# Kernel tuning notes

Measured on AMD Instinct MI355X. Metric: run time of the kernel, lower is better.

Reference implementation:

```python
import jax, jax.numpy as jnp
import numpy as np

T, B, N, M, H, I = 64, 256, 256, 128, 1024, 128
S = 3  # 2*shift_range + 1
EPS = 1e-8  # torch cosine_similarity eps


def setup_inputs() -> dict:
    key = jax.random.key(0)
    ks = jax.random.split(key, 24)
    def rn(k, shp, scale):
        return (jax.random.normal(k, shp) * scale).astype(jnp.float32)
    sH = 1.0 / np.sqrt(H)
    sC = 1.0 / np.sqrt(I + M)
    sM = 1.0 / np.sqrt(M)
    return {
        'x': rn(ks[0], (T, B, I), 1.0),
        # controller (ffnn): Linear(I+M -> H), stored as [in, out]
        'Wc': rn(ks[1], (I + M, H), sC), 'bc': jnp.zeros((H,), jnp.float32),
        # head params stacked: index 0 = write head, 1 = read head
        'Wk': rn(ks[2], (2, H, M), sH), 'bk': jnp.zeros((2, M), jnp.float32),
        'Wb': rn(ks[3], (2, H, 1), sH), 'bb': jnp.zeros((2, 1), jnp.float32),
        'Wg': rn(ks[4], (2, H, 1), sH), 'bg': jnp.zeros((2, 1), jnp.float32),
        'Ws': rn(ks[5], (2, H, S), sH), 'bs': jnp.zeros((2, S), jnp.float32),
        'Wgam': rn(ks[6], (2, H, 1), sH), 'bgam': jnp.zeros((2, 1), jnp.float32),
        'We': rn(ks[7], (H, M), sH), 'be': jnp.zeros((M,), jnp.float32),
        'Wa': rn(ks[8], (H, M), sH), 'ba': rn(ks[9], (M,), 1.0),
        'Wo': rn(ks[10], (M, I), sM), 'bo': jnp.zeros((I,), jnp.float32),
        # learned initial state
        'memory0': rn(ks[11], (1, N, M), 0.05),
        'ww0': rn(ks[12], (1, N), 0.05),
        'rw0': rn(ks[13], (1, N), 0.05),
        'read0': rn(ks[14], (1, M), 0.05),
    }


def reference(x, Wc, bc, Wk, bk, Wb, bb, Wg, bg, Ws, bs, Wgam, bgam,
              We, be, Wa, ba, Wo, bo, memory0, ww0, rw0, read0):
    Bb = x.shape[1]
    Nn = memory0.shape[1]

    def head(i, ht, memory, prev_w):
        k = jax.nn.relu(ht @ Wk[i] + bk[i])                      # [B, M]
        beta = jax.nn.softplus(ht @ Wb[i] + bb[i])               # [B, 1]
        g = jax.nn.sigmoid(ht @ Wg[i] + bg[i])                   # [B, 1]
        shift = jax.nn.softmax(ht @ Ws[i] + bs[i], axis=1)       # [B, S]
        gamma = jax.nn.relu(ht @ Wgam[i] + bgam[i]) + 1.0        # [B, 1]
        # content addressing: cosine similarity then sharpened softmax
        kn = jnp.maximum(jnp.linalg.norm(k, axis=-1, keepdims=True), EPS)   # [B,1]
        mn = jnp.maximum(jnp.linalg.norm(memory, axis=-1), EPS)             # [B,N]
        cos = jnp.einsum('bm,bnm->bn', k, memory) / (kn * mn)
        w = jax.nn.softmax(beta * cos, axis=1)
        # interpolation with previous weight
        w = g * w + (1.0 - g) * prev_w
        # circular convolutional shift (kernel size S=3, cross-correlation like F.conv1d)
        pad = jnp.concatenate([w[:, -1:], w, w[:, :1]], axis=1)  # [B, N+2]
        w = sum(shift[:, j:j + 1] * pad[:, j:j + Nn] for j in range(S))
        # sharpening
        w = w ** gamma
        return w / jnp.sum(w, axis=1, keepdims=True)

    mem = jnp.tile(memory0, (Bb, 1, 1))
    ww = jax.nn.softmax(jnp.tile(ww0, (Bb, 1)), axis=1)
    rw = jax.nn.softmax(jnp.tile(rw0, (Bb, 1)), axis=1)
    rd = jnp.tile(read0, (Bb, 1))

    def step(carry, xt):
        memory, ww, rw, rd = carry
        inp = jnp.concatenate([xt, rd], axis=1)
        ht = jnp.tanh(inp @ Wc + bc)                             # ffnn controller
        ww = head(0, ht, memory, ww)                             # write head
        rw = head(1, ht, memory, rw)                             # read head
        erase = jax.nn.sigmoid(ht @ We + be)                     # [B, M]
        add = jax.nn.sigmoid(ht @ Wa + ba)                       # [B, M]
        memory = memory * (1.0 - ww[:, :, None] * erase[:, None, :]) \
                 + ww[:, :, None] * add[:, None, :]
        rd = jnp.einsum('bn,bnm->bm', rw, memory)
        out = rd @ Wo + bo
        return (memory, ww, rw, rd), out

    _, ys = jax.lax.scan(step, (mem, ww, rw, rd), x)
    return ys  # [T, B, I]
```

## Files before the change

### kernel.cpp

```cpp
#include <hip/hip_runtime.h>
#include <math.h>

#define T_ 64
#define B_ 256
#define N_ 256
#define M_ 128
#define H_ 1024
#define I_ 128
#define NB 256
#define NT 512
#define MSTR 132
#define EPSF 1e-8f

#define WS_WCR  0
#define WS_W2V  131072
#define WS_WSM  (131072 + 262144)

typedef _Float16 h2_t __attribute__((ext_vector_type(2)));

__device__ __forceinline__ float fdot2(unsigned a, unsigned b, float c) {
#if __has_builtin(__builtin_amdgcn_fdot2)
  union { unsigned u; h2_t h; } ua, ub;
  ua.u = a; ub.u = b;
  return __builtin_amdgcn_fdot2(ua.h, ub.h, c, false);
#else
  union { unsigned u; _Float16 h[2]; } ua, ub;
  ua.u = a; ub.u = b;
  return c + (float)ua.h[0] * (float)ub.h[0] + (float)ua.h[1] * (float)ub.h[1];
#endif
}

__device__ __forceinline__ unsigned packh2(float a, float b) {
  union { h2_t h; unsigned u; } v;
  v.h = h2_t{(_Float16)a, (_Float16)b};
  return v.u;
}

__device__ __forceinline__ float wave_rsum(float v) {
#pragma unroll
  for (int o = 32; o > 0; o >>= 1) v += __shfl_xor(v, o, 64);
  return v;
}
__device__ __forceinline__ float wave_rmax(float v) {
#pragma unroll
  for (int o = 32; o > 0; o >>= 1) v = fmaxf(v, __shfl_xor(v, o, 64));
  return v;
}

__global__ void ntm_pack(const float* __restrict__ Wc, const float* __restrict__ Wk,
                         const float* __restrict__ Wb, const float* __restrict__ Wg,
                         const float* __restrict__ Wsf, const float* __restrict__ Wgm,
                         const float* __restrict__ We, const float* __restrict__ Wa,
                         unsigned* __restrict__ wsu)
{
  const int total = 131072 + 262144 + 6144;
  for (int i = blockIdx.x * blockDim.x + threadIdx.x; i < total;
       i += gridDim.x * blockDim.x) {
    if (i < 131072) {
      int u = i;
      int k8 = u >> 12, rem = u & 4095, h = rem >> 2, jm = rem & 3;
      int j = k8 * 4 + jm;
      wsu[WS_WCR + u] = packh2(Wc[(size_t)j * H_ + h], Wc[(size_t)(j + 128) * H_ + h]);
    } else if (i < 131072 + 262144) {
      int u = i - 131072;
      int k8 = u >> 11, rem = u & 2047, c = rem >> 2, jm = rem & 3;
      int h = k8 * 4 + jm;
      float v0, v1;
      if (c < 128)      { v0 = Wk[(size_t)h * M_ + c];             v1 = Wk[(size_t)(h + 512) * M_ + c]; }
      else if (c < 256) { v0 = Wk[(size_t)H_ * M_ + (size_t)h * M_ + (c - 128)];
                          v1 = Wk[(size_t)H_ * M_ + (size_t)(h + 512) * M_ + (c - 128)]; }
      else if (c < 384) { v0 = We[(size_t)h * M_ + (c - 256)];     v1 = We[(size_t)(h + 512) * M_ + (c - 256)]; }
      else              { v0 = Wa[(size_t)h * M_ + (c - 384)];     v1 = Wa[(size_t)(h + 512) * M_ + (c - 384)]; }
      wsu[WS_W2V + u] = packh2(v0, v1);
    } else {
      int u = i - 131072 - 262144;
      int d = u >> 9, j = u & 511;
      float v0, v1;
      if (d < 2)      { v0 = Wb[d * H_ + j];        v1 = Wb[d * H_ + j + 512]; }
      else if (d < 4) { v0 = Wg[(d - 2) * H_ + j];  v1 = Wg[(d - 2) * H_ + j + 512]; }
      else if (d < 6) { v0 = Wgm[(d - 4) * H_ + j]; v1 = Wgm[(d - 4) * H_ + j + 512]; }
      else if (d < 9) { v0 = Wsf[j * 3 + (d - 6)];  v1 = Wsf[(j + 512) * 3 + (d - 6)]; }
      else            { v0 = Wsf[3 * H_ + j * 3 + (d - 9)]; v1 = Wsf[3 * H_ + (j + 512) * 3 + (d - 9)]; }
      wsu[WS_WSM + u] = packh2(v0, v1);
    }
  }
}

__global__ __launch_bounds__(NT)
void ntm_main(const float* __restrict__ x,
              const float* __restrict__ bc,  const float* __restrict__ bk,
              const float* __restrict__ bbv, const float* __restrict__ bg,
              const float* __restrict__ bsf, const float* __restrict__ bgm,
              const float* __restrict__ be,  const float* __restrict__ ba,
              const float* __restrict__ Wo,  const float* __restrict__ bo,
              const float* __restrict__ mem0, const float* __restrict__ ww0,
              const float* __restrict__ rw0,  const float* __restrict__ rd0,
              const unsigned* __restrict__ wsu,
              float* __restrict__ out)
{
  __shared__ __align__(16) float mem[N_ * MSTR];
  __shared__ __align__(16) float hts[H_];
  __shared__ __align__(16) unsigned htp[512];
  __shared__ __align__(16) unsigned inpp[128];
  __shared__ __align__(16) float prevw[2 * N_];
  __shared__ __align__(16) float mnv[N_];
  __shared__ __align__(16) float ksh[2 * M_];
  __shared__ __align__(16) float eah[2 * M_];
  __shared__ __align__(16) float wlog[2 * N_];
  __shared__ __align__(16) float wtmp[2 * N_];
  __shared__ __align__(16) float red[2 * N_];
  __shared__ __align__(16) float red2[2 * N_];
  __shared__ __align__(16) float rds[M_];
  __shared__ __align__(16) float scal[32];
  __shared__ __align__(16) float bcL[H_];
  __shared__ __align__(16) float bkL[256];
  __shared__ __align__(16) float beL[128];
  __shared__ __align__(16) float baL[128];
  __shared__ __align__(16) float boL[128];
  __shared__ __align__(16) float sb[16];

  const int tid = threadIdx.x;
  const int b = blockIdx.x;
  const uint4* WcR4 = (const uint4*)(wsu + WS_WCR);
  const uint4* W2v4 = (const uint4*)(wsu + WS_W2V);
  const uint4* Wsm4 = (const uint4*)(wsu + WS_WSM);
  const uint4* ip4 = (const uint4*)inpp;
  const uint4* hp4 = (const uint4*)htp;

  for (int i = tid; i < N_ * M_; i += NT)
    mem[(i >> 7) * MSTR + (i & 127)] = mem0[i];
  for (int i = tid; i < H_; i += NT) bcL[i] = bc[i];
  if (tid < 256) bkL[tid] = bk[tid];
  if (tid < 128) { beL[tid] = be[tid]; baL[tid] = ba[tid]; boL[tid] = bo[tid]; rds[tid] = rd0[tid]; }
  if (tid < 12) {
    float v;
    if (tid < 2) v = bbv[tid];
    else if (tid < 4) v = bg[tid - 2];
    else if (tid < 6) v = bgm[tid - 4];
    else v = bsf[tid - 6];
    sb[tid] = v;
  }
  if (tid < 256) { wlog[tid] = ww0[tid]; wlog[256 + tid] = rw0[tid]; }
  __syncthreads();
  if (tid < 256) {
    float s = 0.f;
#pragma unroll 8
    for (int m = 0; m < M_; ++m) { float v = mem[tid * MSTR + m]; s += v * v; }
    mnv[tid] = fmaxf(sqrtf(s), EPSF);
  }
  __syncthreads();
  {
    int wv = tid >> 6, ln = tid & 63;
    if (wv < 2) {
      float l0 = wlog[wv * N_ + ln], l1 = wlog[wv * N_ + 64 + ln],
            l2 = wlog[wv * N_ + 128 + ln], l3 = wlog[wv * N_ + 192 + ln];
      float mx = wave_rmax(fmaxf(fmaxf(l0, l1), fmaxf(l2, l3)));
      float e0 = __expf(l0 - mx), e1 = __expf(l1 - mx), e2 = __expf(l2 - mx), e3 = __expf(l3 - mx);
      float sm = wave_rsum(e0 + e1 + e2 + e3);
      wlog[wv * N_ + ln] = e0; wlog[wv * N_ + 64 + ln] = e1;
      wlog[wv * N_ + 128 + ln] = e2; wlog[wv * N_ + 192 + ln] = e3;
      if (ln == 0) scal[30 + wv] = 1.f / sm;
    }
  }
  __syncthreads();
  prevw[tid] = wlog[tid] * scal[30 + (tid >> 8)];
  if (tid < 128) inpp[tid] = packh2(x[(size_t)b * I_ + tid], rds[tid]);
  __syncthreads();

  for (int t = 0; t < T_; ++t) {
    {
      const int j = tid;
      float a0 = 0.f, a1 = 0.f;
#pragma unroll 8
      for (int k8 = 0; k8 < 32; ++k8) {
        uint4 wa = WcR4[k8 * 1024 + j];
        uint4 wb = WcR4[k8 * 1024 + 512 + j];
        uint4 ip = ip4[k8];
        a0 = fdot2(wa.x, ip.x, a0); a0 = fdot2(wa.y, ip.y, a0);
        a0 = fdot2(wa.z, ip.z, a0); a0 = fdot2(wa.w, ip.w, a0);
        a1 = fdot2(wb.x, ip.x, a1); a1 = fdot2(wb.y, ip.y, a1);
        a1 = fdot2(wb.z, ip.z, a1); a1 = fdot2(wb.w, ip.w, a1);
      }
      float t0 = tanhf(a0 + bcL[j]);
      float t1 = tanhf(a1 + bcL[j + 512]);
      hts[j] = t0; hts[j + 512] = t1;
      htp[j] = packh2(t0, t1);
    }
    __syncthreads();

    {
      const int j = tid;
      float acc = 0.f;
#pragma unroll 8
      for (int k8 = 0; k8 < 128; ++k8) {
        uint4 wv = W2v4[k8 * 512 + j];
        uint4 hv = hp4[k8];
        acc = fdot2(wv.x, hv.x, acc); acc = fdot2(wv.y, hv.y, acc);
        acc = fdot2(wv.z, hv.z, acc); acc = fdot2(wv.w, hv.w, acc);
      }
      if (j < 256)      ksh[j] = fmaxf(acc + bkL[j], 0.f);
      else if (j < 384) eah[j - 256] = 1.f / (1.f + __expf(-(acc + beL[j - 256])));
      else              eah[j - 256] = 1.f / (1.f + __expf(-(acc + baL[j - 384])));
    }
    __syncthreads();

    {
      int wv = tid >> 6, ln = tid & 63;
      if (wv < 6) {
        for (int dd = 0; dd < 2; ++dd) {
          int d = wv * 2 + dd;
          uint4 wA = Wsm4[d * 128 + ln * 2];
          uint4 wB = Wsm4[d * 128 + ln * 2 + 1];
          uint4 hA = hp4[ln * 2];
          uint4 hB = hp4[ln * 2 + 1];
          float s = 0.f;
          s = fdot2(wA.x, hA.x, s); s = fdot2(wA.y, hA.y, s);
          s = fdot2(wA.z, hA.z, s); s = fdot2(wA.w, hA.w, s);
          s = fdot2(wB.x, hB.x, s); s = fdot2(wB.y, hB.y, s);
          s = fdot2(wB.z, hB.z, s); s = fdot2(wB.w, hB.w, s);
          s = wave_rsum(s);
          if (ln == 0) scal[d] = s;
        }
      } else if (wv < 8) {
        int h = wv - 6;
        float v0 = ksh[h * 128 + ln], v1 = ksh[h * 128 + 64 + ln];
        float s = wave_rsum(v0 * v0 + v1 * v1);
        if (ln == 0) scal[12 + h] = fmaxf(sqrtf(s), EPSF);
      }
    }
    __syncthreads();

    if (tid == 0) {
      for (int h = 0; h < 2; ++h) {
        float rb = scal[h] + sb[h];
        scal[16 + h] = (rb > 20.f) ? rb : log1pf(__expf(rb));
        scal[18 + h] = 1.f / (1.f + __expf(-(scal[2 + h] + sb[2 + h])));
        scal[20 + h] = fmaxf(scal[4 + h] + sb[4 + h], 0.f) + 1.f;
        float s0 = scal[6 + 3 * h] + sb[6 + 3 * h];
        float s1 = scal[7 + 3 * h] + sb[7 + 3 * h];
        float s2 = scal[8 + 3 * h] + sb[8 + 3 * h];
        float mx = fmaxf(s0, fmaxf(s1, s2));
        float e0 = __expf(s0 - mx), e1 = __expf(s1 - mx), e2 = __expf(s2 - mx);
        float inv = 1.f / (e0 + e1 + e2);
        scal[22 + 3 * h] = e0 * inv; scal[23 + 3 * h] = e1 * inv; scal[24 + 3 * h] = e2 * inv;
      }
    }
    __syncthreads();

    {
      int wv = tid >> 6, ln = tid & 63;
      int h = wv & 1, n = (wv >> 1) * 64 + ln;
      const float beta = scal[16 + h], kn = scal[12 + h];
      const float4* kp = (const float4*)&ksh[h * 128];
      const float* mrow = &mem[n * MSTR];
      float dot = 0.f;
#pragma unroll 8
      for (int m4 = 0; m4 < 32; ++m4) {
        float4 kv = kp[m4];
        float4 mv = *(const float4*)&mrow[m4 * 4];
        dot += kv.x * mv.x + kv.y * mv.y + kv.z * mv.z + kv.w * mv.w;
      }
      wlog[h * N_ + n] = beta * (dot / (kn * mnv[n]));
    }
    __syncthreads();

    {
      int wv = tid >> 6, ln = tid & 63;
      if (wv < 2) {
        float l0 = wlog[wv * N_ + ln], l1 = wlog[wv * N_ + 64 + ln],
              l2 = wlog[wv * N_ + 128 + ln], l3 = wlog[wv * N_ + 192 + ln];
        float mx = wave_rmax(fmaxf(fmaxf(l0, l1), fmaxf(l2, l3)));
        float e0 = __expf(l0 - mx), e1 = __expf(l1 - mx), e2 = __expf(l2 - mx), e3 = __expf(l3 - mx);
        float sm = wave_rsum(e0 + e1 + e2 + e3);
        wlog[wv * N_ + ln] = e0; wlog[wv * N_ + 64 + ln] = e1;
        wlog[wv * N_ + 128 + ln] = e2; wlog[wv * N_ + 192 + ln] = e3;
        if (ln == 0) scal[30 + wv] = 1.f / sm;
      }
    }
    __syncthreads();

    {
      int h = tid >> 8;
      float g = scal[18 + h];
      wtmp[tid] = g * wlog[tid] * scal[30 + h] + (1.f - g) * prevw[tid];
    }
    __syncthreads();

    {
      int h = tid >> 8, n = tid & 255;
      float v = scal[22 + 3 * h] * wtmp[h * N_ + ((n + 255) & 255)]
              + scal[23 + 3 * h] * wtmp[h * N_ + n]
              + scal[24 + 3 * h] * wtmp[h * N_ + ((n + 1) & 255)];
      wlog[tid] = __powf(v, scal[20 + h]);
    }
    __syncthreads();

    {
      int wv = tid >> 6, ln = tid & 63;
      if (wv < 2) {
        float s = wlog[wv * N_ + ln] + wlog[wv * N_ + 64 + ln]
                + wlog[wv * N_ + 128 + ln] + wlog[wv * N_ + 192 + ln];
        s = wave_rsum(s);
        if (ln == 0) scal[14 + wv] = 1.f / s;
      }
    }
    __syncthreads();

    prevw[tid] = wlog[tid] * scal[14 + (tid >> 8)];
    __syncthreads();

    {
      int n = tid & 255, half = tid >> 8;
      float wwn = prevw[n];
      float* mrow = &mem[n * MSTR + half * 64];
      const float4* ep = (const float4*)&eah[half * 64];
      const float4* ap = (const float4*)&eah[128 + half * 64];
      float sq = 0.f;
#pragma unroll 4
      for (int m4 = 0; m4 < 16; ++m4) {
        float4 mv = *(float4*)&mrow[m4 * 4];
        float4 ev = ep[m4], av = ap[m4];
        mv.x = mv.x * (1.f - wwn * ev.x) + wwn * av.x;
        mv.y = mv.y * (1.f - wwn * ev.y) + wwn * av.y;
        mv.z = mv.z * (1.f - wwn * ev.z) + wwn * av.z;
        mv.w = mv.w * (1.f - wwn * ev.w) + wwn * av.w;
        sq += mv.x * mv.x + mv.y * mv.y + mv.z * mv.z + mv.w * mv.w;
        *(float4*)&mrow[m4 * 4] = mv;
      }
      red[half * N_ + n] = sq;
    }
    __syncthreads();

    if (tid < 256) mnv[tid] = fmaxf(sqrtf(red[tid] + red[N_ + tid]), EPSF);
    {
      int m = tid & 127, g = tid >> 7;
      float acc = 0.f;
      const float* base = &mem[(g * 64) * MSTR + m];
#pragma unroll 4
      for (int i = 0; i < 64; ++i)
        acc += prevw[N_ + g * 64 + i] * base[i * MSTR];
      red2[g * 128 + m] = acc;
    }
    __syncthreads();

    if (tid < 128)
      rds[tid] = red2[tid] + red2[128 + tid] + red2[256 + tid] + red2[384 + tid];
    __syncthreads();

    {
      int c = tid & 127, q = tid >> 7;
      int m0 = q * 32;
      float acc = 0.f;
#pragma unroll 8
      for (int mm = 0; mm < 32; ++mm)
        acc += rds[m0 + mm] * Wo[(size_t)(m0 + mm) * I_ + c];
      red[q * 128 + c] = acc;
    }
    __syncthreads();

    if (tid < 128) {
      float v = red[tid] + red[128 + tid] + red[256 + tid] + red[384 + tid] + boL[tid];
      out[((size_t)t * B_ + b) * I_ + tid] = v;
      if (t < T_ - 1)
        inpp[tid] = packh2(x[((size_t)(t + 1) * B_ + b) * I_ + tid], rds[tid]);
    }
    __syncthreads();
  }
}

extern "C" void kernel_launch(void* const* d_in, const int* in_sizes, int n_in,
                              void* d_out, int out_size, void* d_ws, size_t ws_size,
                              hipStream_t stream) {
  (void)in_sizes; (void)n_in; (void)out_size; (void)ws_size;

  const float* x    = (const float*)d_in[0];
  const float* Wc   = (const float*)d_in[1];
  const float* bc   = (const float*)d_in[2];
  const float* Wk   = (const float*)d_in[3];
  const float* bk   = (const float*)d_in[4];
  const float* Wb   = (const float*)d_in[5];
  const float* bbv  = (const float*)d_in[6];
  const float* Wg   = (const float*)d_in[7];
  const float* bg   = (const float*)d_in[8];
  const float* Wsf  = (const float*)d_in[9];
  const float* bsf  = (const float*)d_in[10];
  const float* Wgm  = (const float*)d_in[11];
  const float* bgm  = (const float*)d_in[12];
  const float* We   = (const float*)d_in[13];
  const float* be   = (const float*)d_in[14];
  const float* Wa   = (const float*)d_in[15];
  const float* ba   = (const float*)d_in[16];
  const float* Wo   = (const float*)d_in[17];
  const float* bo   = (const float*)d_in[18];
  const float* mem0 = (const float*)d_in[19];
  const float* ww0  = (const float*)d_in[20];
  const float* rw0  = (const float*)d_in[21];
  const float* rd0  = (const float*)d_in[22];
  float* out = (float*)d_out;
  unsigned* wsu = (unsigned*)d_ws;

  ntm_pack<<<dim3(512), dim3(256), 0, stream>>>(Wc, Wk, Wb, Wg, Wsf, Wgm, We, Wa, wsu);
  ntm_main<<<dim3(NB), dim3(NT), 0, stream>>>(x, bc, bk, bbv, bg, bsf, bgm, be, ba,
                                              Wo, bo, mem0, ww0, rw0, rd0, wsu, out);
}
```

Baseline: 1.465 ms.

## Precompute x-projection in separate kernel, double threads, restructure per-step phases

The x half of the controller matmul is hoisted into a batched pre-kernel that writes fp16 results to workspace, used only when the workspace is large enough; otherwise the old in-loop path runs. The main kernel moves to 1024 threads per block and re-lays out the weights as k-contiguous per-output rows. The Wo output projection is deferred into the next step's controller phase, the shift/scalar dot products are merged with the gate stage, and several barriers are fused. Costs include higher register pressure at 1024 threads, fp16 rounding of the precomputed x term, and correctness that depends on the workspace size.

Result: slower. 4.981 ms (+240.1%).

```diff
diff --git a/kernel.cpp b/kernel.cpp
--- a/kernel.cpp
+++ b/kernel.cpp
@@ -8,34 +8,35 @@
 #define H_ 1024
 #define I_ 128
 #define NB 256
-#define NT 512
+#define NT 1024
 #define MSTR 132
 #define EPSF 1e-8f
 
-#define WS_WCR  0
-#define WS_W2V  131072
-#define WS_WSM  (131072 + 262144)
+#define WS_WCX 0
+#define WS_WCR 65536
+#define WS_W2P 131072
+#define WS_WOP 393216
+#define WS_WSM 401408
+#define WS_XC  407552
+#define WS_BYTES_NEEDED ((size_t)(407552 + 8388608) * 4)
 
 typedef _Float16 h2_t __attribute__((ext_vector_type(2)));
 
 __device__ __forceinline__ float fdot2(unsigned a, unsigned b, float c) {
-#if __has_builtin(__builtin_amdgcn_fdot2)
   union { unsigned u; h2_t h; } ua, ub;
   ua.u = a; ub.u = b;
   return __builtin_amdgcn_fdot2(ua.h, ub.h, c, false);
-#else
-  union { unsigned u; _Float16 h[2]; } ua, ub;
-  ua.u = a; ub.u = b;
-  return c + (float)ua.h[0] * (float)ub.h[0] + (float)ua.h[1] * (float)ub.h[1];
-#endif
-}
-
+}
 __device__ __forceinline__ unsigned packh2(float a, float b) {
   union { h2_t h; unsigned u; } v;
   v.h = h2_t{(_Float16)a, (_Float16)b};
   return v.u;
 }
-
+__device__ __forceinline__ float dot4(uint4 w, uint4 h, float acc) {
+  acc = fdot2(w.x, h.x, acc); acc = fdot2(w.y, h.y, acc);
+  acc = fdot2(w.z, h.z, acc); acc = fdot2(w.w, h.w, acc);
+  return acc;
+}
 __device__ __forceinline__ float wave_rsum(float v) {
 #pragma unroll
   for (int o = 32; o > 0; o >>= 1) v += __shfl_xor(v, o, 64);
@@ -51,38 +52,74 @@
                          const float* __restrict__ Wb, const float* __restrict__ Wg,
                          const float* __restrict__ Wsf, const float* __restrict__ Wgm,
                          const float* __restrict__ We, const float* __restrict__ Wa,
+                         const float* __restrict__ Wo,
                          unsigned* __restrict__ wsu)
 {
-  const int total = 131072 + 262144 + 6144;
+  const int total = 65536 + 65536 + 262144 + 8192 + 6144;
   for (int i = blockIdx.x * blockDim.x + threadIdx.x; i < total;
        i += gridDim.x * blockDim.x) {
-    if (i < 131072) {
-      int u = i;
-      int k8 = u >> 12, rem = u & 4095, h = rem >> 2, jm = rem & 3;
-      int j = k8 * 4 + jm;
-      wsu[WS_WCR + u] = packh2(Wc[(size_t)j * H_ + h], Wc[(size_t)(j + 128) * H_ + h]);
+    if (i < 65536) {
+      int h = i >> 6, k2 = i & 63;
+      wsu[WS_WCX + i] = packh2(Wc[(size_t)(2 * k2) * H_ + h], Wc[(size_t)(2 * k2 + 1) * H_ + h]);
+    } else if (i < 131072) {
+      int u = i - 65536, h = u >> 6, k2 = u & 63;
+      wsu[WS_WCR + u] = packh2(Wc[(size_t)(128 + 2 * k2) * H_ + h],
+                               Wc[(size_t)(129 + 2 * k2) * H_ + h]);
     } else if (i < 131072 + 262144) {
-      int u = i - 131072;
-      int k8 = u >> 11, rem = u & 2047, c = rem >> 2, jm = rem & 3;
-      int h = k8 * 4 + jm;
+      int u = i - 131072, c = u >> 9, k2 = u & 511;
+      int k0 = 2 * k2, k1 = 2 * k2 + 1;
       float v0, v1;
-      if (c < 128)      { v0 = Wk[(size_t)h * M_ + c];             v1 = Wk[(size_t)(h + 512) * M_ + c]; }
-      else if (c < 256) { v0 = Wk[(size_t)H_ * M_ + (size_t)h * M_ + (c - 128)];
-                          v1 = Wk[(size_t)H_ * M_ + (size_t)(h + 512) * M_ + (c - 128)]; }
-      else if (c < 384) { v0 = We[(size_t)h * M_ + (c - 256)];     v1 = We[(size_t)(h + 512) * M_ + (c - 256)]; }
-      else              { v0 = Wa[(size_t)h * M_ + (c - 384)];     v1 = Wa[(size_t)(h + 512) * M_ + (c - 384)]; }
-      wsu[WS_W2V + u] = packh2(v0, v1);
+      if (c < 128)      { v0 = Wk[(size_t)k0 * M_ + c];           v1 = Wk[(size_t)k1 * M_ + c]; }
+      else if (c < 256) { v0 = Wk[(size_t)H_ * M_ + (size_t)k0 * M_ + (c - 128)];
+                          v1 = Wk[(size_t)H_ * M_ + (size_t)k1 * M_ + (c - 128)]; }
+      else if (c < 384) { v0 = We[(size_t)k0 * M_ + (c - 256)];   v1 = We[(size_t)k1 * M_ + (c - 256)]; }
+      else              { v0 = Wa[(size_t)k0 * M_ + (c - 384)];   v1 = Wa[(size_t)k1 * M_ + (c - 384)]; }
+      wsu[WS_W2P + u] = packh2(v0, v1);
+    } else if (i < 131072 + 262144 + 8192) {
+      int u = i - 131072 - 262144, c = u >> 6, m2 = u & 63;
+      wsu[WS_WOP + u] = packh2(Wo[(size_t)(2 * m2) * I_ + c], Wo[(size_t)(2 * m2 + 1) * I_ + c]);
     } else {
-      int u = i - 131072 - 262144;
-      int d = u >> 9, j = u & 511;
+      int u = i - 131072 - 262144 - 8192, d = u >> 9, k2 = u & 511;
+      int k0 = 2 * k2, k1 = 2 * k2 + 1;
       float v0, v1;
-      if (d < 2)      { v0 = Wb[d * H_ + j];        v1 = Wb[d * H_ + j + 512]; }
-      else if (d < 4) { v0 = Wg[(d - 2) * H_ + j];  v1 = Wg[(d - 2) * H_ + j + 512]; }
-      else if (d < 6) { v0 = Wgm[(d - 4) * H_ + j]; v1 = Wgm[(d - 4) * H_ + j + 512]; }
-      else if (d < 9) { v0 = Wsf[j * 3 + (d - 6)];  v1 = Wsf[(j + 512) * 3 + (d - 6)]; }
-      else            { v0 = Wsf[3 * H_ + j * 3 + (d - 9)]; v1 = Wsf[3 * H_ + (j + 512) * 3 + (d - 9)]; }
+      if (d < 2)      { v0 = Wb[d * H_ + k0];        v1 = Wb[d * H_ + k1]; }
+      else if (d < 4) { v0 = Wg[(d - 2) * H_ + k0];  v1 = Wg[(d - 2) * H_ + k1]; }
+      else if (d < 6) { v0 = Wgm[(d - 4) * H_ + k0]; v1 = Wgm[(d - 4) * H_ + k1]; }
+      else if (d < 9) { v0 = Wsf[k0 * 3 + (d - 6)];  v1 = Wsf[k1 * 3 + (d - 6)]; }
+      else            { v0 = Wsf[3 * H_ + k0 * 3 + (d - 9)]; v1 = Wsf[3 * H_ + k1 * 3 + (d - 9)]; }
       wsu[WS_WSM + u] = packh2(v0, v1);
     }
+  }
+}
+
+__global__ __launch_bounds__(256)
+void ntm_xc(const float* __restrict__ x, const unsigned* __restrict__ wsu,
+            unsigned* __restrict__ wsout)
+{
+  __shared__ __align__(16) _Float16 xt[16 * 128];
+  const int tid = threadIdx.x;
+  const size_t row0 = (size_t)blockIdx.x * 16;
+  for (int i = tid; i < 16 * 128; i += 256)
+    xt[i] = (_Float16)x[(row0 + (i >> 7)) * I_ + (i & 127)];
+  __syncthreads();
+  _Float16* xc16 = (_Float16*)(wsout + WS_XC);
+  const uint4* xt4 = (const uint4*)xt;
+  for (int cq = 0; cq < 4; ++cq) {
+    const int col = cq * 256 + tid;
+    const uint4* w4 = (const uint4*)(wsu + WS_WCX) + col * 16;
+    float acc[16];
+#pragma unroll
+    for (int r = 0; r < 16; ++r) acc[r] = 0.f;
+#pragma unroll 4
+    for (int k4 = 0; k4 < 16; ++k4) {
+      uint4 w = w4[k4];
+#pragma unroll
+      for (int r = 0; r < 16; ++r)
+        acc[r] = dot4(w, xt4[r * 16 + k4], acc[r]);
+    }
+#pragma unroll
+    for (int r = 0; r < 16; ++r)
+      xc16[(row0 + r) * H_ + col] = (_Float16)acc[r];
   }
 }
 
@@ -92,25 +129,24 @@
               const float* __restrict__ bbv, const float* __restrict__ bg,
               const float* __restrict__ bsf, const float* __restrict__ bgm,
               const float* __restrict__ be,  const float* __restrict__ ba,
-              const float* __restrict__ Wo,  const float* __restrict__ bo,
+              const float* __restrict__ bo,
               const float* __restrict__ mem0, const float* __restrict__ ww0,
               const float* __restrict__ rw0,  const float* __restrict__ rd0,
               const unsigned* __restrict__ wsu,
-              float* __restrict__ out)
+              float* __restrict__ out, int useXc)
 {
   __shared__ __align__(16) float mem[N_ * MSTR];
-  __shared__ __align__(16) float hts[H_];
-  __shared__ __align__(16) unsigned htp[512];
-  __shared__ __align__(16) unsigned inpp[128];
+  __shared__ __align__(16) _Float16 ht16[H_];
+  __shared__ __align__(16) _Float16 rd16[M_];
+  __shared__ __align__(16) _Float16 x16[M_];
   __shared__ __align__(16) float prevw[2 * N_];
   __shared__ __align__(16) float mnv[N_];
   __shared__ __align__(16) float ksh[2 * M_];
   __shared__ __align__(16) float eah[2 * M_];
   __shared__ __align__(16) float wlog[2 * N_];
   __shared__ __align__(16) float wtmp[2 * N_];
-  __shared__ __align__(16) float red[2 * N_];
-  __shared__ __align__(16) float red2[2 * N_];
-  __shared__ __align__(16) float rds[M_];
+  __shared__ __align__(16) float redU[2048];
+  __shared__ __align__(16) float sdots[24];
   __shared__ __align__(16) float scal[32];
   __shared__ __align__(16) float bcL[H_];
   __shared__ __align__(16) float bkL[256];
@@ -121,17 +157,13 @@
 
   const int tid = threadIdx.x;
   const int b = blockIdx.x;
-  const uint4* WcR4 = (const uint4*)(wsu + WS_WCR);
-  const uint4* W2v4 = (const uint4*)(wsu + WS_W2V);
-  const uint4* Wsm4 = (const uint4*)(wsu + WS_WSM);
-  const uint4* ip4 = (const uint4*)inpp;
-  const uint4* hp4 = (const uint4*)htp;
+  const _Float16* xcg = (const _Float16*)(wsu + WS_XC);
 
   for (int i = tid; i < N_ * M_; i += NT)
     mem[(i >> 7) * MSTR + (i & 127)] = mem0[i];
-  for (int i = tid; i < H_; i += NT) bcL[i] = bc[i];
+  bcL[tid] = bc[tid];
   if (tid < 256) bkL[tid] = bk[tid];
-  if (tid < 128) { beL[tid] = be[tid]; baL[tid] = ba[tid]; boL[tid] = bo[tid]; rds[tid] = rd0[tid]; }
+  if (tid < 128) { beL[tid] = be[tid]; baL[tid] = ba[tid]; boL[tid] = bo[tid]; }
   if (tid < 12) {
     float v;
     if (tid < 2) v = bbv[tid];
@@ -140,7 +172,7 @@
     else v = bsf[tid - 6];
     sb[tid] = v;
   }
-  if (tid < 256) { wlog[tid] = ww0[tid]; wlog[256 + tid] = rw0[tid]; }
+  if (tid < 512) wlog[tid] = (tid < 256) ? ww0[tid] : rw0[tid - 256];
   __syncthreads();
   if (tid < 256) {
     float s = 0.f;
@@ -148,7 +180,6 @@
     for (int m = 0; m < M_; ++m) { float v = mem[tid * MSTR + m]; s += v * v; }
     mnv[tid] = fmaxf(sqrtf(s), EPSF);
   }
-  __syncthreads();
   {
     int wv = tid >> 6, ln = tid & 63;
     if (wv < 2) {
@@ -163,66 +194,107 @@
     }
   }
   __syncthreads();
-  prevw[tid] = wlog[tid] * scal[30 + (tid >> 8)];
-  if (tid < 128) inpp[tid] = packh2(x[(size_t)b * I_ + tid], rds[tid]);
+  if (tid < 512) prevw[tid] = wlog[tid] * scal[30 + (tid >> 8)];
+  if (tid < 64)
+    ((unsigned*)rd16)[tid] = packh2(rd0[2 * tid], rd0[2 * tid + 1]);
+  if (!useXc && tid >= 64 && tid < 128) {
+    int k = tid - 64;
+    ((unsigned*)x16)[k] = packh2(x[(size_t)b * I_ + 2 * k], x[(size_t)b * I_ + 2 * k + 1]);
+  }
   __syncthreads();
 
   for (int t = 0; t < T_; ++t) {
     {
       const int j = tid;
-      float a0 = 0.f, a1 = 0.f;
-#pragma unroll 8
-      for (int k8 = 0; k8 < 32; ++k8) {
-        uint4 wa = WcR4[k8 * 1024 + j];
-        uint4 wb = WcR4[k8 * 1024 + 512 + j];
-        uint4 ip = ip4[k8];
-        a0 = fdot2(wa.x, ip.x, a0); a0 = fdot2(wa.y, ip.y, a0);
-        a0 = fdot2(wa.z, ip.z, a0); a0 = fdot2(wa.w, ip.w, a0);
-        a1 = fdot2(wb.x, ip.x, a1); a1 = fdot2(wb.y, ip.y, a1);
-        a1 = fdot2(wb.z, ip.z, a1); a1 = fdot2(wb.w, ip.w, a1);
-      }
-      float t0 = tanhf(a0 + bcL[j]);
-      float t1 = tanhf(a1 + bcL[j + 512]);
-      hts[j] = t0; hts[j + 512] = t1;
-      htp[j] = packh2(t0, t1);
-    }
-    __syncthreads();
-
-    {
-      const int j = tid;
-      float acc = 0.f;
-#pragma unroll 8
-      for (int k8 = 0; k8 < 128; ++k8) {
-        uint4 wv = W2v4[k8 * 512 + j];
-        uint4 hv = hp4[k8];
-        acc = fdot2(wv.x, hv.x, acc); acc = fdot2(wv.y, hv.y, acc);
-        acc = fdot2(wv.z, hv.z, acc); acc = fdot2(wv.w, hv.w, acc);
-      }
-      if (j < 256)      ksh[j] = fmaxf(acc + bkL[j], 0.f);
-      else if (j < 384) eah[j - 256] = 1.f / (1.f + __expf(-(acc + beL[j - 256])));
-      else              eah[j - 256] = 1.f / (1.f + __expf(-(acc + baL[j - 384])));
-    }
-    __syncthreads();
-
-    {
-      int wv = tid >> 6, ln = tid & 63;
-      if (wv < 6) {
-        for (int dd = 0; dd < 2; ++dd) {
-          int d = wv * 2 + dd;
-          uint4 wA = Wsm4[d * 128 + ln * 2];
-          uint4 wB = Wsm4[d * 128 + ln * 2 + 1];
-          uint4 hA = hp4[ln * 2];
-          uint4 hB = hp4[ln * 2 + 1];
-          float s = 0.f;
-          s = fdot2(wA.x, hA.x, s); s = fdot2(wA.y, hA.y, s);
-          s = fdot2(wA.z, hA.z, s); s = fdot2(wA.w, hA.w, s);
-          s = fdot2(wB.x, hB.x, s); s = fdot2(wB.y, hB.y, s);
-          s = fdot2(wB.z, hB.z, s); s = fdot2(wB.w, hB.w, s);
+      float acc;
+      if (useXc) {
+        acc = (float)xcg[((size_t)t * B_ + b) * H_ + j];
+      } else {
+        acc = 0.f;
+        const uint4* wx = (const uint4*)(wsu + WS_WCX) + j * 16;
+        const uint4* xp4 = (const uint4*)x16;
+#pragma unroll 4
+        for (int k4 = 0; k4 < 16; ++k4) acc = dot4(wx[k4], xp4[k4], acc);
+      }
+      const uint4* wr = (const uint4*)(wsu + WS_WCR) + j * 16;
+      const uint4* rp4 = (const uint4*)rd16;
+#pragma unroll 4
+      for (int k4 = 0; k4 < 16; ++k4) acc = dot4(wr[k4], rp4[k4], acc);
+      ht16[j] = (_Float16)tanhf(acc + bcL[j]);
+      if (t > 0) {
+        int c = tid & 127, q = tid >> 7;
+        const uint4* wo4 = (const uint4*)(wsu + WS_WOP) + c * 16 + q * 2;
+        const uint4* rq4 = ((const uint4*)rd16) + q * 2;
+        float s = dot4(wo4[0], rq4[0], 0.f);
+        s = dot4(wo4[1], rq4[1], s);
+        redU[1024 + q * 128 + c] = s;
+      }
+    }
+    __syncthreads();
+
+    {
+      const int c = tid & 511, half = tid >> 9;
+      const uint4* w4 = (const uint4*)(wsu + WS_W2P) + c * 128 + half * 64;
+      const uint4* h4 = ((const uint4*)ht16) + half * 64;
+      float a0 = 0.f, a1 = 0.f, a2 = 0.f, a3 = 0.f;
+#pragma unroll 2
+      for (int k4 = 0; k4 < 64; k4 += 4) {
+        a0 = dot4(w4[k4],     h4[k4],     a0);
+        a1 = dot4(w4[k4 + 1], h4[k4 + 1], a1);
+        a2 = dot4(w4[k4 + 2], h4[k4 + 2], a2);
+        a3 = dot4(w4[k4 + 3], h4[k4 + 3], a3);
+      }
+      redU[half * 512 + c] = (a0 + a1) + (a2 + a3);
+      if (tid < 128 && t > 0) {
+        float o = boL[tid];
+#pragma unroll
+        for (int q = 0; q < 8; ++q) o += redU[1024 + q * 128 + tid];
+        out[((size_t)(t - 1) * B_ + b) * I_ + tid] = o;
+      }
+    }
+    __syncthreads();
+
+    {
+      if (tid < 512) {
+        float v = redU[tid] + redU[512 + tid];
+        if (tid < 256)      ksh[tid] = fmaxf(v + bkL[tid], 0.f);
+        else if (tid < 384) eah[tid - 256] = 1.f / (1.f + __expf(-(v + beL[tid - 256])));
+        else                eah[tid - 256] = 1.f / (1.f + __expf(-(v + baL[tid - 384])));
+      } else {
+        int wv = (tid >> 6) - 8, ln = tid & 63;
+#pragma unroll
+        for (int i = 0; i < 3; ++i) {
+          int hd = wv * 3 + i;
+          int d = hd >> 1, half = hd & 1;
+          const uint4* wp = (const uint4*)(wsu + WS_WSM) + d * 128 + half * 64;
+          float s = dot4(wp[ln], ((const uint4*)ht16)[half * 64 + ln], 0.f);
           s = wave_rsum(s);
-          if (ln == 0) scal[d] = s;
+          if (ln == 0) sdots[hd] = s;
         }
-      } else if (wv < 8) {
-        int h = wv - 6;
+      }
+    }
+    __syncthreads();
+
+    {
+      if (tid == 0) {
+        for (int h = 0; h < 2; ++h) {
+          float Sb = sdots[2 * h] + sdots[2 * h + 1];
+          float Sg = sdots[2 * (2 + h)] + sdots[2 * (2 + h) + 1];
+          float Sgm = sdots[2 * (4 + h)] + sdots[2 * (4 + h) + 1];
+          float rb = Sb + sb[h];
+          scal[16 + h] = (rb > 20.f) ? rb : log1pf(__expf(rb));
+          scal[18 + h] = 1.f / (1.f + __expf(-(Sg + sb[2 + h])));
+          scal[20 + h] = fmaxf(Sgm + sb[4 + h], 0.f) + 1.f;
+          float s0 = sdots[2 * (6 + 3 * h)] + sdots[2 * (6 + 3 * h) + 1] + sb[6 + 3 * h];
+          float s1 = sdots[2 * (7 + 3 * h)] + sdots[2 * (7 + 3 * h) + 1] + sb[7 + 3 * h];
+          float s2 = sdots[2 * (8 + 3 * h)] + sdots[2 * (8 + 3 * h) + 1] + sb[8 + 3 * h];
+          float mx = fmaxf(s0, fmaxf(s1, s2));
+          float e0 = __expf(s0 - mx), e1 = __expf(s1 - mx), e2 = __expf(s2 - mx);
+          float inv = 1.f / (e0 + e1 + e2);
+          scal[22 + 3 * h] = e0 * inv; scal[23 + 3 * h] = e1 * inv; scal[24 + 3 * h] = e2 * inv;
+        }
+      } else if (tid >= 64 && tid < 192) {
+        int h = (tid >> 6) - 1, ln = tid & 63;
         float v0 = ksh[h * 128 + ln], v1 = ksh[h * 128 + 64 + ln];
         float s = wave_rsum(v0 * v0 + v1 * v1);
         if (ln == 0) scal[12 + h] = fmaxf(sqrtf(s), EPSF);
@@ -230,37 +302,19 @@
     }
     __syncthreads();
 
-    if (tid == 0) {
-      for (int h = 0; h < 2; ++h) {
-        float rb = scal[h] + sb[h];
-        scal[16 + h] = (rb > 20.f) ? rb : log1pf(__expf(rb));
-        scal[18 + h] = 1.f / (1.f + __expf(-(scal[2 + h] + sb[2 + h])));
-        scal[20 + h] = fmaxf(scal[4 + h] + sb[4 + h], 0.f) + 1.f;
-        float s0 = scal[6 + 3 * h] + sb[6 + 3 * h];
-        float s1 = scal[7 + 3 * h] + sb[7 + 3 * h];
-        float s2 = scal[8 + 3 * h] + sb[8 + 3 * h];
-        float mx = fmaxf(s0, fmaxf(s1, s2));
-        float e0 = __expf(s0 - mx), e1 = __expf(s1 - mx), e2 = __expf(s2 - mx);
-        float inv = 1.f / (e0 + e1 + e2);
-        scal[22 + 3 * h] = e0 * inv; scal[23 + 3 * h] = e1 * inv; scal[24 + 3 * h] = e2 * inv;
-      }
-    }
-    __syncthreads();
-
-    {
-      int wv = tid >> 6, ln = tid & 63;
-      int h = wv & 1, n = (wv >> 1) * 64 + ln;
-      const float beta = scal[16 + h], kn = scal[12 + h];
-      const float4* kp = (const float4*)&ksh[h * 128];
-      const float* mrow = &mem[n * MSTR];
+    {
+      int half = tid & 1, r = (tid >> 1) & 255, h = tid >> 9;
+      const float4* kp = (const float4*)&ksh[h * 128 + half * 64];
+      const float4* mp = (const float4*)&mem[r * MSTR + half * 64];
       float dot = 0.f;
-#pragma unroll 8
-      for (int m4 = 0; m4 < 32; ++m4) {
-        float4 kv = kp[m4];
-        float4 mv = *(const float4*)&mrow[m4 * 4];
+#pragma unroll
+      for (int i = 0; i < 16; ++i) {
+        float4 kv = kp[i], mv = mp[i];
         dot += kv.x * mv.x + kv.y * mv.y + kv.z * mv.z + kv.w * mv.w;
       }
-      wlog[h * N_ + n] = beta * (dot / (kn * mnv[n]));
+      dot += __shfl_xor(dot, 1, 64);
+      if (half == 0)
+        wlog[h * 256 + r] = scal[16 + h] * (dot / (scal[12 + h] * mnv[r]));
     }
     __syncthreads();
 
@@ -279,14 +333,14 @@
     }
     __syncthreads();
 
-    {
+    if (tid < 512) {
       int h = tid >> 8;
       float g = scal[18 + h];
       wtmp[tid] = g * wlog[tid] * scal[30 + h] + (1.f - g) * prevw[tid];
     }
     __syncthreads();
 
-    {
+    if (tid < 512) {
       int h = tid >> 8, n = tid & 255;
       float v = scal[22 + 3 * h] * wtmp[h * N_ + ((n + 255) & 255)]
               + scal[23 + 3 * h] * wtmp[h * N_ + n]
@@ -306,72 +360,86 @@
     }
     __syncthreads();
 
-    prevw[tid] = wlog[tid] * scal[14 + (tid >> 8)];
-    __syncthreads();
-
-    {
-      int n = tid & 255, half = tid >> 8;
-      float wwn = prevw[n];
-      float* mrow = &mem[n * MSTR + half * 64];
-      const float4* ep = (const float4*)&eah[half * 64];
-      const float4* ap = (const float4*)&eah[128 + half * 64];
+    {
+      int n = tid & 255, q = tid >> 8;
+      float wwn = wlog[n] * scal[14];
+      float* mrow = &mem[n * MSTR + q * 32];
+      const float4* ep = (const float4*)&eah[q * 32];
+      const float4* ap = (const float4*)&eah[128 + q * 32];
       float sq = 0.f;
-#pragma unroll 4
-      for (int m4 = 0; m4 < 16; ++m4) {
-        float4 mv = *(float4*)&mrow[m4 * 4];
-        float4 ev = ep[m4], av = ap[m4];
+#pragma unroll
+      for (int i = 0; i < 8; ++i) {
+        float4 mv = *(float4*)&mrow[i * 4];
+        float4 ev = ep[i], av = ap[i];
         mv.x = mv.x * (1.f - wwn * ev.x) + wwn * av.x;
         mv.y = mv.y * (1.f - wwn * ev.y) + wwn * av.y;
         mv.z = mv.z * (1.f - wwn * ev.z) + wwn * av.z;
         mv.w = mv.w * (1.f - wwn * ev.w) + wwn * av.w;
         sq += mv.x * mv.x + mv.y * mv.y + mv.z * mv.z + mv.w * mv.w;
-        *(float4*)&mrow[m4 * 4] = mv;
-      }
-      red[half * N_ + n] = sq;
-    }
-    __syncthreads();
-
-    if (tid < 256) mnv[tid] = fmaxf(sqrtf(red[tid] + red[N_ + tid]), EPSF);
+        *(float4*)&mrow[i * 4] = mv;
+      }
+      redU[1024 + q * 256 + n] = sq;
+      if (q == 0) prevw[n] = wwn;
+    }
+    __syncthreads();
+
     {
       int m = tid & 127, g = tid >> 7;
-      float acc = 0.f;
-      const float* base = &mem[(g * 64) * MSTR + m];
-#pragma unroll 4
-      for (int i = 0; i < 64; ++i)
-        acc += prevw[N_ + g * 64 + i] * base[i * MSTR];
-      red2[g * 128 + m] = acc;
-    }
-    __syncthreads();
-
-    if (tid < 128)
-      rds[tid] = red2[tid] + red2[128 + tid] + red2[256 + tid] + red2[384 + tid];
-    __syncthreads();
-
-    {
-      int c = tid & 127, q = tid >> 7;
-      int m0 = q * 32;
+      const float* basep = &mem[g * 32 * MSTR + m];
       float acc = 0.f;
 #pragma unroll 8
-      for (int mm = 0; mm < 32; ++mm)
-        acc += rds[m0 + mm] * Wo[(size_t)(m0 + mm) * I_ + c];
-      red[q * 128 + c] = acc;
-    }
-    __syncthreads();
-
-    if (tid < 128) {
-      float v = red[tid] + red[128 + tid] + red[256 + tid] + red[384 + tid] + boL[tid];
-      out[((size_t)t * B_ + b) * I_ + tid] = v;
-      if (t < T_ - 1)
-        inpp[tid] = packh2(x[((size_t)(t + 1) * B_ + b) * I_ + tid], rds[tid]);
-    }
-    __syncthreads();
+      for (int i = 0; i < 32; ++i)
+        acc += wlog[256 + g * 32 + i] * basep[i * MSTR];
+      redU[g * 128 + m] = acc;
+    }
+    __syncthreads();
+
+    {
+      if (tid < 64) {
+        float r0 = 0.f, r1 = 0.f;
+#pragma unroll
+        for (int g = 0; g < 8; ++g) {
+          r0 += redU[g * 128 + 2 * tid];
+          r1 += redU[g * 128 + 2 * tid + 1];
+        }
+        ((unsigned*)rd16)[tid] = packh2(r0 * scal[15], r1 * scal[15]);
+      } else if (tid >= 256 && tid < 512) {
+        int n = tid - 256;
+        prevw[256 + n] = wlog[256 + n] * scal[15];
+      } else if (tid >= 512 && tid < 768) {
+        int n = tid - 512;
+        float s = redU[1024 + n] + redU[1280 + n] + redU[1536 + n] + redU[1792 + n];
+        mnv[n] = fmaxf(sqrtf(s), EPSF);
+      } else if (!useXc && tid >= 768 && tid < 832 && t < T_ - 1) {
+        int k = tid - 768;
+        const float* xr = &x[((size_t)(t + 1) * B_ + b) * I_];
+        ((unsigned*)x16)[k] = packh2(xr[2 * k], xr[2 * k + 1]);
+      }
+    }
+    __syncthreads();
+  }
+
+  {
+    int c = tid & 127, q = tid >> 7;
+    const uint4* wo4 = (const uint4*)(wsu + WS_WOP) + c * 16 + q * 2;
+    const uint4* rq4 = ((const uint4*)rd16) + q * 2;
+    float s = dot4(wo4[0], rq4[0], 0.f);
+    s = dot4(wo4[1], rq4[1], s);
+    redU[1024 + q * 128 + c] = s;
+  }
+  __syncthreads();
+  if (tid < 128) {
+    float o = boL[tid];
+#pragma unroll
+    for (int q = 0; q < 8; ++q) o += redU[1024 + q * 128 + tid];
+    out[((size_t)(T_ - 1) * B_ + b) * I_ + tid] = o;
   }
 }
 
 extern "C" void kernel_launch(void* const* d_in, const int* in_sizes, int n_in,
                               void* d_out, int out_size, void* d_ws, size_t ws_size,
                               hipStream_t stream) {
-  (void)in_sizes; (void)n_in; (void)out_size; (void)ws_size;
+  (void)in_sizes; (void)n_in; (void)out_size;
 
   const float* x    = (const float*)d_in[0];
   const float* Wc   = (const float*)d_in[1];
@@ -399,7 +467,11 @@
   float* out = (float*)d_out;
   unsigned* wsu = (unsigned*)d_ws;
 
-  ntm_pack<<<dim3(512), dim3(256), 0, stream>>>(Wc, Wk, Wb, Wg, Wsf, Wgm, We, Wa, wsu);
-  ntm_main<<<dim3(NB), dim3(NT), 0, stream>>>(x, bc, bk, bbv, bg, bsf, bgm, be, ba,
-                                              Wo, bo, mem0, ww0, rw0, rd0, wsu, out);
-}
+  const int useXc = (ws_size >= WS_BYTES_NEEDED) ? 1 : 0;
+
+  ntm_pack<<<dim3(512), dim3(256), 0, stream>>>(Wc, Wk, Wb, Wg, Wsf, Wgm, We, Wa, Wo, wsu);
+  if (useXc)
+    ntm_xc<<<dim3(T_ * B_ / 16), dim3(256), 0, stream>>>(x, wsu, wsu);
+  ntm_main<<<dim3(NB), dim3(NT), 0, stream>>>(x, bc, bk, bbv, bg, bsf, bgm, be, ba, bo,
+                                              mem0, ww0, rw0, rd0, wsu, out, useXc);
+}
```
